# Optimization experiments

Measured on AMD Instinct MI355X. Metric: run time of the kernel, lower is better.

The kernel has to match this reference:

```python
import jax, jax.numpy as jnp
import numpy as np

COMMITMENT_COST = 0.25


def setup_inputs() -> dict:
    key = jax.random.key(0)
    k1, k2 = jax.random.split(key)
    n_embeddings, embedding_dim = 1024, 256
    x = jax.random.normal(k1, (32, 2048, embedding_dim), dtype=jnp.float32)
    r = 1.0 / n_embeddings
    embedding = jax.random.uniform(k2, (n_embeddings, embedding_dim),
                                   dtype=jnp.float32, minval=-r, maxval=r)
    return {"x": x, "embedding": embedding}


def reference(x, embedding):
    M, D = embedding.shape
    # x is detached before flattening in the original quantize()
    x_flat = jax.lax.stop_gradient(x).reshape(-1, D)  # [N, D]
    distances = (jnp.sum(embedding * embedding, axis=1)
                 + jnp.sum(x_flat * x_flat, axis=1, keepdims=True)
                 - 2.0 * (x_flat @ embedding.T))  # [N, M]
    indices = jnp.argmin(distances, axis=-1)  # [N] int
    quantized = embedding[indices].reshape(x.shape)  # gather + view_as(x)
    # commitment loss: quantized is detached in the loss term
    e_latent_loss = jnp.mean(jnp.square(x - jax.lax.stop_gradient(quantized)))
    loss = COMMITMENT_COST * e_latent_loss
    return quantized, loss, indices
```

## Files before the change

kernel.cpp:

```cpp
#include <hip/hip_runtime.h>

#define N_ROWS   65536
#define D        256
#define D4       64
#define M        1024
#define LOSS_OFF 16777216
#define IDX_OFF  16777217
#define COMMIT_SCALE (0.25f / 16777216.0f)
#define E_SCALE  1024.0f
#define C_SCALE  0.001953125f

typedef _Float16 f16x8 __attribute__((ext_vector_type(8)));
typedef _Float16 f16x4 __attribute__((ext_vector_type(4)));
typedef float    f32x4 __attribute__((ext_vector_type(4)));

__device__ __forceinline__ void async_copy16(const void* g, void* l) {
    __builtin_amdgcn_global_load_lds(
        (const __attribute__((address_space(1))) unsigned int*)g,
        (__attribute__((address_space(3))) unsigned int*)l, 16, 0, 0);
}

__device__ __forceinline__ float np_block128(const float* __restrict__ a, int l) {
    float r0 = __fmul_rn(a[l +   0], a[l +   0]);
    float r1 = __fmul_rn(a[l +  16], a[l +  16]);
    float r2 = __fmul_rn(a[l +  32], a[l +  32]);
    float r3 = __fmul_rn(a[l +  48], a[l +  48]);
    float r4 = __fmul_rn(a[l +  64], a[l +  64]);
    float r5 = __fmul_rn(a[l +  80], a[l +  80]);
    float r6 = __fmul_rn(a[l +  96], a[l +  96]);
    float r7 = __fmul_rn(a[l + 112], a[l + 112]);
    return __fadd_rn(__fadd_rn(__fadd_rn(r0, r1), __fadd_rn(r2, r3)),
                     __fadd_rn(__fadd_rn(r4, r5), __fadd_rn(r6, r7)));
}
__device__ __forceinline__ float np_reduce16(float v) {
    float s = __fadd_rn(v, __shfl_down(v, 8));
    s = __fadd_rn(s, __shfl_down(s, 4));
    s = __fadd_rn(s, __shfl_down(s, 2));
    s = __fadd_rn(s, __shfl_down(s, 1));
    return s;
}

__global__ __launch_bounds__(256) void norms_kernel(
    const float4* __restrict__ x4, const float4* __restrict__ emb4,
    float* __restrict__ bsq, float* __restrict__ esq,
    float* __restrict__ loss_slot) {
    __shared__ float rowbuf[16 * 260];
    const int tid = threadIdx.x;
    const float4* src4;
    float* dst;
    int row0;
    if (blockIdx.x < 4096) {
        row0 = blockIdx.x * 16;
        src4 = x4 + (size_t)row0 * 64;
        dst = bsq + row0;
    } else {
        row0 = (blockIdx.x - 4096) * 16;
        src4 = emb4 + (size_t)row0 * 64;
        dst = esq + row0;
    }
    #pragma unroll
    for (int p = 0; p < 4; ++p) {
        const int f = tid + p * 256;
        const int r = f >> 6, c4 = f & 63;
        *(float4*)&rowbuf[r * 260 + c4 * 4] = src4[f];
    }
    __syncthreads();
    const int l = tid & 15, g = tid >> 4;
    const float* base = &rowbuf[g * 260];
    const float v0 = np_block128(base, l);
    const float v1 = np_block128(base + 128, l);
    const float t0 = np_reduce16(v0);
    const float t1 = np_reduce16(v1);
    if (l == 0) dst[g] = __fadd_rn(t0, t1);
    if (blockIdx.x == 0 && tid == 0) *loss_slot = 0.0f;
}

__global__ __launch_bounds__(256) void esplit_kernel(
    const float4* __restrict__ emb4,
    _Float16* __restrict__ e_hi, _Float16* __restrict__ e_mid) {
    const int f = blockIdx.x * 256 + threadIdx.x;
    const int code = f >> 6, k4 = f & 63;
    const int kc = k4 >> 3, k8 = k4 & 7;
    const int q = k8 >> 1, half = k8 & 1;
    const int jt = code >> 7, cl = code & 127;
    const int cg = cl >> 4, lmc = cl & 15;
    float4 v = emb4[f];
    float a[4] = {v.x * E_SCALE, v.y * E_SCALE, v.z * E_SCALE, v.w * E_SCALE};
    f16x4 hi, mid;
    #pragma unroll
    for (int j = 0; j < 4; ++j) {
        _Float16 h = (_Float16)a[j];
        float r = __fsub_rn(a[j], (float)h);
        hi[j] = h;
        mid[j] = (_Float16)r;
    }
    const size_t ofs = (size_t)kc * 32768 + (size_t)jt * 4096
                     + (size_t)(cg * 64 + q * 16 + lmc) * 8 + half * 4;
    *(f16x4*)&e_hi[ofs]  = hi;
    *(f16x4*)&e_mid[ofs] = mid;
}

__global__ __launch_bounds__(256, 2) void argmin_mfma_kernel(
    const float* __restrict__ x,
    const _Float16* __restrict__ e_hi, const _Float16* __restrict__ e_mid,
    const float* __restrict__ esq, const float* __restrict__ bsq,
    float* __restrict__ idx_out_f, int* __restrict__ idx_out_i) {
    __shared__ __attribute__((aligned(16))) _Float16 buf[2][8192];
    __shared__ float red_d[64][2];
    __shared__ int   red_i[64][2];

    const int tid = threadIdx.x;
    const int w = tid >> 6, lane = tid & 63;
    const int w_row = w >> 1, w_col = w & 1;
    const int lm = lane & 15, q = lane >> 4;
    const int row0 = blockIdx.x * 64;

    f16x8 a_hi[2][8], a_mid[2][8];
    #pragma unroll
    for (int fm = 0; fm < 2; ++fm) {
        const float* xr = x + (size_t)(row0 + w_row * 32 + fm * 16 + lm) * D + q * 8;
        #pragma unroll
        for (int kc = 0; kc < 8; ++kc) {
            float4 v0 = *(const float4*)(xr + kc * 32);
            float4 v1 = *(const float4*)(xr + kc * 32 + 4);
            float e[8] = {v0.x, v0.y, v0.z, v0.w, v1.x, v1.y, v1.z, v1.w};
            #pragma unroll
            for (int j = 0; j < 8; ++j) {
                _Float16 h = (_Float16)e[j];
                float r = __fsub_rn(e[j], (float)h);
                a_hi[fm][kc][j]  = h;
                a_mid[fm][kc][j] = (_Float16)r;
            }
        }
    }
    float bq[2][4];
    #pragma unroll
    for (int fm = 0; fm < 2; ++fm)
        #pragma unroll
        for (int r = 0; r < 4; ++r)
            bq[fm][r] = bsq[row0 + w_row * 32 + fm * 16 + q * 4 + r];

    float best[2][4] = {{3.0e38f, 3.0e38f, 3.0e38f, 3.0e38f},
                        {3.0e38f, 3.0e38f, 3.0e38f, 3.0e38f}};
    int bidx[2][4] = {{0, 0, 0, 0}, {0, 0, 0, 0}};

    auto dma = [&](int c, int bsel) {
        const int jt = c >> 3, kc = c & 7;
        const size_t gofs = (size_t)kc * 65536 + (size_t)jt * 8192
                          + (size_t)w * 2048 + (size_t)lane * 16;
        const char* gh = (const char*)e_hi + gofs;
        const char* gm = (const char*)e_mid + gofs;
        _Float16* lh = &buf[bsel][w * 1024];
        _Float16* lmm = &buf[bsel][4096 + w * 1024];
        async_copy16(gh, lh);
        async_copy16(gh + 1024, lh + 512);
        async_copy16(gm, lmm);
        async_copy16(gm + 1024, lmm + 512);
    };

    dma(0, 0);
    for (int jt = 0; jt < 8; ++jt) {
        const int j0 = jt * 128;
        f32x4 acc[2][4] = {};
        for (int kc = 0; kc < 8; ++kc) {
            const int c = jt * 8 + kc;
            __syncthreads();
            if (c < 63) dma(c + 1, (c + 1) & 1);
            const int bsel = c & 1;
            f16x8 bh[4], bm[4];
            const int lofs = lane * 8;
            #pragma unroll
            for (int fn = 0; fn < 4; ++fn) {
                const int bo = (w_col * 4 + fn) * 512 + lofs;
                bh[fn] = *(const f16x8*)&buf[bsel][bo];
                bm[fn] = *(const f16x8*)&buf[bsel][4096 + bo];
            }
            #pragma unroll
            for (int fm = 0; fm < 2; ++fm)
                #pragma unroll
                for (int fn = 0; fn < 4; ++fn) {
                    acc[fm][fn] = __builtin_amdgcn_mfma_f32_16x16x32_f16(
                        a_hi[fm][kc], bh[fn], acc[fm][fn], 0, 0, 0);
                    acc[fm][fn] = __builtin_amdgcn_mfma_f32_16x16x32_f16(
                        a_mid[fm][kc], bh[fn], acc[fm][fn], 0, 0, 0);
                    acc[fm][fn] = __builtin_amdgcn_mfma_f32_16x16x32_f16(
                        a_hi[fm][kc], bm[fn], acc[fm][fn], 0, 0, 0);
                }
        }
        #pragma unroll
        for (int fn = 0; fn < 4; ++fn) {
            const int j = j0 + w_col * 64 + fn * 16 + lm;
            const float eq = esq[j];
            #pragma unroll
            for (int fm = 0; fm < 2; ++fm)
                #pragma unroll
                for (int r = 0; r < 4; ++r) {
                    const float d = __fsub_rn(__fadd_rn(eq, bq[fm][r]),
                                              acc[fm][fn][r] * C_SCALE);
                    if (d < best[fm][r]) { best[fm][r] = d; bidx[fm][r] = j; }
                }
        }
    }
    #pragma unroll
    for (int fm = 0; fm < 2; ++fm)
        #pragma unroll
        for (int r = 0; r < 4; ++r) {
            float d = best[fm][r]; int i = bidx[fm][r];
            #pragma unroll
            for (int mv = 1; mv <= 8; mv <<= 1) {
                const float d2 = __shfl_xor(d, mv, 64);
                const int   i2 = __shfl_xor(i, mv, 64);
                if (d2 < d || (d2 == d && i2 < i)) { d = d2; i = i2; }
            }
            best[fm][r] = d; bidx[fm][r] = i;
        }
    __syncthreads();
    if (lm == 0) {
        #pragma unroll
        for (int fm = 0; fm < 2; ++fm)
            #pragma unroll
            for (int r = 0; r < 4; ++r) {
                const int rl = w_row * 32 + fm * 16 + q * 4 + r;
                red_d[rl][w_col] = best[fm][r];
                red_i[rl][w_col] = bidx[fm][r];
            }
    }
    __syncthreads();
    if (tid < 64) {
        float d0 = red_d[tid][0]; int i0 = red_i[tid][0];
        const float d1 = red_d[tid][1]; const int i1 = red_i[tid][1];
        if (d1 < d0 || (d1 == d0 && i1 < i0)) { d0 = d1; i0 = i1; }
        idx_out_f[row0 + tid] = (float)i0;
        idx_out_i[row0 + tid] = i0;
    }
}

__global__ __launch_bounds__(256) void gather_loss_kernel(
    const float4* __restrict__ x4, const float4* __restrict__ emb4,
    const int* __restrict__ idx, float4* __restrict__ q4,
    float* __restrict__ loss_slot) {
    const int base = blockIdx.x * 256 + threadIdx.x;
    float acc = 0.0f;
    #pragma unroll
    for (int i = 0; i < 16; ++i) {
        const int f   = base + i * (1024 * 256);
        const int row = f >> 6;
        const int c4  = f & 63;
        const int e   = idx[row];
        float4 qv = emb4[e * D4 + c4];
        float4 xv = x4[f];
        q4[f] = qv;
        const float dx = xv.x - qv.x, dy = xv.y - qv.y;
        const float dz = xv.z - qv.z, dw = xv.w - qv.w;
        acc += dx * dx + dy * dy + dz * dz + dw * dw;
    }
    #pragma unroll
    for (int off = 32; off; off >>= 1) acc += __shfl_down(acc, off, 64);
    __shared__ float wsum[4];
    const int lane = threadIdx.x & 63, w = threadIdx.x >> 6;
    if (lane == 0) wsum[w] = acc;
    __syncthreads();
    if (threadIdx.x == 0) {
        atomicAdd(loss_slot, (wsum[0] + wsum[1] + wsum[2] + wsum[3]) * COMMIT_SCALE);
    }
}

extern "C" void kernel_launch(void* const* d_in, const int* in_sizes, int n_in,
                              void* d_out, int out_size, void* d_ws, size_t ws_size,
                              hipStream_t stream) {
    const float* x   = (const float*)d_in[0];
    const float* emb = (const float*)d_in[1];
    float* out = (float*)d_out;
    float*    bsq  = (float*)d_ws;
    float*    esq  = bsq + N_ROWS;
    int*      idx  = (int*)(esq + M);
    _Float16* e_hi = (_Float16*)(idx + N_ROWS);
    _Float16* e_mid = e_hi + (size_t)M * D;

    norms_kernel<<<4096 + M / 16, 256, 0, stream>>>((const float4*)x,
                                                    (const float4*)emb,
                                                    bsq, esq, out + LOSS_OFF);
    esplit_kernel<<<M * D / 4 / 256, 256, 0, stream>>>((const float4*)emb,
                                                       e_hi, e_mid);
    argmin_mfma_kernel<<<N_ROWS / 64, 256, 0, stream>>>(x, e_hi, e_mid,
                                                        esq, bsq,
                                                        out + IDX_OFF, idx);
    gather_loss_kernel<<<1024, 256, 0, stream>>>((const float4*)x,
                                                 (const float4*)emb, idx,
                                                 (float4*)out, out + LOSS_OFF);
}
```

Measured before the change: 248.5 us.

## Triple-buffer codebook DMA with explicit vmcnt waits and stage esq in LDS

Moves the codebook tile prefetch from double to triple buffering, so chunk c+2 is issued while chunk c is computed. The __syncthreads is replaced by explicit s_waitcnt vmcnt(4)/s_barrier sequences so only the oldest DMA must complete before each step. MFMA blocks are raised in wave priority with s_setprio, and the esq table is staged in LDS instead of being read from global memory in the epilogue. The extra buffer increases LDS use, which may limit occupancy, and the hand-written waitcnt logic relies on an exact count of outstanding loads.

```diff
diff --git a/kernel.cpp b/kernel.cpp
--- a/kernel.cpp
+++ b/kernel.cpp
@@ -105,7 +105,8 @@
     const _Float16* __restrict__ e_hi, const _Float16* __restrict__ e_mid,
     const float* __restrict__ esq, const float* __restrict__ bsq,
     float* __restrict__ idx_out_f, int* __restrict__ idx_out_i) {
-    __shared__ __attribute__((aligned(16))) _Float16 buf[2][8192];
+    __shared__ __attribute__((aligned(16))) _Float16 buf[3][8192];
+    __shared__ float esq_lds[1024];
     __shared__ float red_d[64][2];
     __shared__ int   red_i[64][2];
 
@@ -115,6 +116,20 @@
     const int lm = lane & 15, q = lane >> 4;
     const int row0 = blockIdx.x * 64;
 
+    auto dma = [&](int c, int s) {
+        const int jt = c >> 3, kc = c & 7;
+        const size_t gofs = (size_t)kc * 65536 + (size_t)jt * 8192
+                          + (size_t)w * 2048 + (size_t)lane * 16;
+        const char* gh = (const char*)e_hi + gofs;
+        const char* gm = (const char*)e_mid + gofs;
+        _Float16* lh = &buf[s][w * 1024];
+        _Float16* lmm = &buf[s][4096 + w * 1024];
+        async_copy16(gh, lh);
+        async_copy16(gh + 1024, lh + 512);
+        async_copy16(gm, lmm);
+        async_copy16(gm + 1024, lmm + 512);
+    };
+
     f16x8 a_hi[2][8], a_mid[2][8];
     #pragma unroll
     for (int fm = 0; fm < 2; ++fm) {
@@ -140,41 +155,43 @@
         for (int r = 0; r < 4; ++r)
             bq[fm][r] = bsq[row0 + w_row * 32 + fm * 16 + q * 4 + r];
 
+    *(float4*)&esq_lds[tid * 4] = ((const float4*)esq)[tid];
+
+    asm volatile("s_waitcnt vmcnt(0)" ::: "memory");
+
+    dma(0, 0);
+    dma(1, 1);
+
     float best[2][4] = {{3.0e38f, 3.0e38f, 3.0e38f, 3.0e38f},
                         {3.0e38f, 3.0e38f, 3.0e38f, 3.0e38f}};
     int bidx[2][4] = {{0, 0, 0, 0}, {0, 0, 0, 0}};
 
-    auto dma = [&](int c, int bsel) {
-        const int jt = c >> 3, kc = c & 7;
-        const size_t gofs = (size_t)kc * 65536 + (size_t)jt * 8192
-                          + (size_t)w * 2048 + (size_t)lane * 16;
-        const char* gh = (const char*)e_hi + gofs;
-        const char* gm = (const char*)e_mid + gofs;
-        _Float16* lh = &buf[bsel][w * 1024];
-        _Float16* lmm = &buf[bsel][4096 + w * 1024];
-        async_copy16(gh, lh);
-        async_copy16(gh + 1024, lh + 512);
-        async_copy16(gm, lmm);
-        async_copy16(gm + 1024, lmm + 512);
-    };
-
-    dma(0, 0);
+    int rslot = 0;
     for (int jt = 0; jt < 8; ++jt) {
         const int j0 = jt * 128;
         f32x4 acc[2][4] = {};
         for (int kc = 0; kc < 8; ++kc) {
             const int c = jt * 8 + kc;
-            __syncthreads();
-            if (c < 63) dma(c + 1, (c + 1) & 1);
-            const int bsel = c & 1;
+            if (c < 63)
+                asm volatile("s_waitcnt vmcnt(4) lgkmcnt(0)\n\t"
+                             "s_barrier" ::: "memory");
+            else
+                asm volatile("s_waitcnt vmcnt(0) lgkmcnt(0)\n\t"
+                             "s_barrier" ::: "memory");
+            __builtin_amdgcn_sched_barrier(0);
+            if (c <= 61) {
+                int ws = rslot + 2; if (ws >= 3) ws -= 3;
+                dma(c + 2, ws);
+            }
             f16x8 bh[4], bm[4];
             const int lofs = lane * 8;
             #pragma unroll
             for (int fn = 0; fn < 4; ++fn) {
                 const int bo = (w_col * 4 + fn) * 512 + lofs;
-                bh[fn] = *(const f16x8*)&buf[bsel][bo];
-                bm[fn] = *(const f16x8*)&buf[bsel][4096 + bo];
-            }
+                bh[fn] = *(const f16x8*)&buf[rslot][bo];
+                bm[fn] = *(const f16x8*)&buf[rslot][4096 + bo];
+            }
+            __builtin_amdgcn_s_setprio(1);
             #pragma unroll
             for (int fm = 0; fm < 2; ++fm)
                 #pragma unroll
@@ -186,11 +203,13 @@
                     acc[fm][fn] = __builtin_amdgcn_mfma_f32_16x16x32_f16(
                         a_hi[fm][kc], bm[fn], acc[fm][fn], 0, 0, 0);
                 }
+            __builtin_amdgcn_s_setprio(0);
+            rslot = (rslot == 2) ? 0 : rslot + 1;
         }
         #pragma unroll
         for (int fn = 0; fn < 4; ++fn) {
             const int j = j0 + w_col * 64 + fn * 16 + lm;
-            const float eq = esq[j];
+            const float eq = esq_lds[j];
             #pragma unroll
             for (int fm = 0; fm < 2; ++fm)
                 #pragma unroll
```

Result: no change. 248.8 us (+0.1%).

## Software-pipeline codebook loads against MFMA and move x-mid fragments to LDS

Applied to the files above, without the earlier changes.

Restructures the argmin MFMA loop so LDS fragment loads for chunk k overlap the MFMAs of chunk k-1, with the distance epilogue deferred and fused into the next tile's first step. The x low-order (mid) fragments move from registers to shared memory, and the codebook norms are staged in LDS. A manual waitcnt plus barrier replaces __syncthreads, and s_setprio raises priority around the MFMA bursts. The aim is to hide LDS and DMA latency and to lower register pressure for occupancy. The cost is extra LDS traffic and footprint, plus hand-placed waits that are fragile.

```diff
diff --git a/kernel.cpp b/kernel.cpp
--- a/kernel.cpp
+++ b/kernel.cpp
@@ -106,101 +106,149 @@
     const float* __restrict__ esq, const float* __restrict__ bsq,
     float* __restrict__ idx_out_f, int* __restrict__ idx_out_i) {
     __shared__ __attribute__((aligned(16))) _Float16 buf[2][8192];
-    __shared__ float red_d[64][2];
-    __shared__ int   red_i[64][2];
+    __shared__ __attribute__((aligned(16))) _Float16 amid[2][8192];
+    __shared__ float esq_lds[1024];
 
     const int tid = threadIdx.x;
     const int w = tid >> 6, lane = tid & 63;
     const int w_row = w >> 1, w_col = w & 1;
     const int lm = lane & 15, q = lane >> 4;
     const int row0 = blockIdx.x * 64;
-
-    f16x8 a_hi[2][8], a_mid[2][8];
-    #pragma unroll
-    for (int fm = 0; fm < 2; ++fm) {
-        const float* xr = x + (size_t)(row0 + w_row * 32 + fm * 16 + lm) * D + q * 8;
-        #pragma unroll
-        for (int kc = 0; kc < 8; ++kc) {
-            float4 v0 = *(const float4*)(xr + kc * 32);
-            float4 v1 = *(const float4*)(xr + kc * 32 + 4);
-            float e[8] = {v0.x, v0.y, v0.z, v0.w, v1.x, v1.y, v1.z, v1.w};
-            #pragma unroll
-            for (int j = 0; j < 8; ++j) {
-                _Float16 h = (_Float16)e[j];
-                float r = __fsub_rn(e[j], (float)h);
-                a_hi[fm][kc][j]  = h;
-                a_mid[fm][kc][j] = (_Float16)r;
-            }
-        }
-    }
-    float bq[2][4];
-    #pragma unroll
-    for (int fm = 0; fm < 2; ++fm)
-        #pragma unroll
-        for (int r = 0; r < 4; ++r)
-            bq[fm][r] = bsq[row0 + w_row * 32 + fm * 16 + q * 4 + r];
-
-    float best[2][4] = {{3.0e38f, 3.0e38f, 3.0e38f, 3.0e38f},
-                        {3.0e38f, 3.0e38f, 3.0e38f, 3.0e38f}};
-    int bidx[2][4] = {{0, 0, 0, 0}, {0, 0, 0, 0}};
-
-    auto dma = [&](int c, int bsel) {
-        const int jt = c >> 3, kc = c & 7;
-        const size_t gofs = (size_t)kc * 65536 + (size_t)jt * 8192
+    const int lofs = lane * 8;
+
+    auto dma = [&](int jtn, int kcn, int s) {
+        const size_t gofs = (size_t)kcn * 65536 + (size_t)jtn * 8192
                           + (size_t)w * 2048 + (size_t)lane * 16;
         const char* gh = (const char*)e_hi + gofs;
         const char* gm = (const char*)e_mid + gofs;
-        _Float16* lh = &buf[bsel][w * 1024];
-        _Float16* lmm = &buf[bsel][4096 + w * 1024];
+        _Float16* lh  = &buf[s][w * 1024];
+        _Float16* lmm = &buf[s][4096 + w * 1024];
         async_copy16(gh, lh);
         async_copy16(gh + 1024, lh + 512);
         async_copy16(gm, lmm);
         async_copy16(gm + 1024, lmm + 512);
     };
 
-    dma(0, 0);
+    dma(0, 0, 0);
+
+    f16x8 a_hi[2][8];
+    #pragma unroll
+    for (int fm = 0; fm < 2; ++fm) {
+        const float* xr = x + (size_t)(row0 + w_row * 32 + fm * 16 + lm) * D + q * 8;
+        #pragma unroll
+        for (int kc = 0; kc < 8; ++kc) {
+            float4 v0 = *(const float4*)(xr + kc * 32);
+            float4 v1 = *(const float4*)(xr + kc * 32 + 4);
+            float e[8] = {v0.x, v0.y, v0.z, v0.w, v1.x, v1.y, v1.z, v1.w};
+            f16x8 hi, md;
+            #pragma unroll
+            for (int j = 0; j < 8; ++j) {
+                _Float16 h = (_Float16)e[j];
+                float r = __fsub_rn(e[j], (float)h);
+                hi[j] = h;
+                md[j] = (_Float16)r;
+            }
+            a_hi[fm][kc] = hi;
+            if (w_col == 0)
+                *(f16x8*)&amid[w_row][(fm * 8 + kc) * 512 + lofs] = md;
+        }
+    }
+    float bq[2][4];
+    #pragma unroll
+    for (int fm = 0; fm < 2; ++fm)
+        #pragma unroll
+        for (int r = 0; r < 4; ++r)
+            bq[fm][r] = bsq[row0 + w_row * 32 + fm * 16 + q * 4 + r];
+
+    *(float4*)&esq_lds[tid * 4] = ((const float4*)esq)[tid];
+
+    asm volatile("s_waitcnt vmcnt(0)" ::: "memory");
+
+    float best[2][4] = {{3.0e38f, 3.0e38f, 3.0e38f, 3.0e38f},
+                        {3.0e38f, 3.0e38f, 3.0e38f, 3.0e38f}};
+    int bidx[2][4] = {{0, 0, 0, 0}, {0, 0, 0, 0}};
+    f32x4 acc[2][4] = {};
+    f16x8 bh[2][4], bm[2][4], am[2][2];
+
+#define MFMA_TRIPLES(P, KCP)                                                  \
+    do {                                                                      \
+        __builtin_amdgcn_s_setprio(1);                                        \
+        _Pragma("unroll")                                                     \
+        for (int fm = 0; fm < 2; ++fm)                                        \
+            _Pragma("unroll")                                                 \
+            for (int fn = 0; fn < 4; ++fn) {                                  \
+                acc[fm][fn] = __builtin_amdgcn_mfma_f32_16x16x32_f16(         \
+                    a_hi[fm][(KCP)], bh[(P)][fn], acc[fm][fn], 0, 0, 0);      \
+                acc[fm][fn] = __builtin_amdgcn_mfma_f32_16x16x32_f16(         \
+                    am[(P)][fm],     bh[(P)][fn], acc[fm][fn], 0, 0, 0);      \
+                acc[fm][fn] = __builtin_amdgcn_mfma_f32_16x16x32_f16(         \
+                    a_hi[fm][(KCP)], bm[(P)][fn], acc[fm][fn], 0, 0, 0);      \
+            }                                                                 \
+        __builtin_amdgcn_s_setprio(0);                                        \
+    } while (0)
+
+#define EPILOGUE(JT)                                                          \
+    do {                                                                      \
+        const int j0e = (JT) * 128;                                           \
+        _Pragma("unroll")                                                     \
+        for (int fn = 0; fn < 4; ++fn) {                                      \
+            const int j = j0e + w_col * 64 + fn * 16 + lm;                    \
+            const float eq = esq_lds[j];                                      \
+            _Pragma("unroll")                                                 \
+            for (int fm = 0; fm < 2; ++fm)                                    \
+                _Pragma("unroll")                                             \
+                for (int r = 0; r < 4; ++r) {                                 \
+                    const float d = __fsub_rn(__fadd_rn(eq, bq[fm][r]),       \
+                                              acc[fm][fn][r] * C_SCALE);      \
+                    if (d < best[fm][r]) { best[fm][r] = d; bidx[fm][r] = j; }\
+                }                                                             \
+        }                                                                     \
+        _Pragma("unroll")                                                     \
+        for (int fm = 0; fm < 2; ++fm)                                        \
+            _Pragma("unroll")                                                 \
+            for (int fn = 0; fn < 4; ++fn)                                    \
+                _Pragma("unroll")                                             \
+                for (int r = 0; r < 4; ++r) acc[fm][fn][r] = 0.0f;            \
+    } while (0)
+
     for (int jt = 0; jt < 8; ++jt) {
-        const int j0 = jt * 128;
-        f32x4 acc[2][4] = {};
+        #pragma unroll
         for (int kc = 0; kc < 8; ++kc) {
-            const int c = jt * 8 + kc;
-            __syncthreads();
-            if (c < 63) dma(c + 1, (c + 1) & 1);
-            const int bsel = c & 1;
-            f16x8 bh[4], bm[4];
-            const int lofs = lane * 8;
-            #pragma unroll
-            for (int fn = 0; fn < 4; ++fn) {
-                const int bo = (w_col * 4 + fn) * 512 + lofs;
-                bh[fn] = *(const f16x8*)&buf[bsel][bo];
-                bm[fn] = *(const f16x8*)&buf[bsel][4096 + bo];
-            }
-            #pragma unroll
-            for (int fm = 0; fm < 2; ++fm)
+            asm volatile("s_waitcnt vmcnt(0) lgkmcnt(0)\n\t"
+                         "s_barrier" ::: "memory");
+            __builtin_amdgcn_sched_barrier(0);
+            if (kc < 7)       dma(jt, kc + 1, (kc + 1) & 1);
+            else if (jt < 7)  dma(jt + 1, 0, 0);
+            {
+                const int P = kc & 1;
                 #pragma unroll
                 for (int fn = 0; fn < 4; ++fn) {
-                    acc[fm][fn] = __builtin_amdgcn_mfma_f32_16x16x32_f16(
-                        a_hi[fm][kc], bh[fn], acc[fm][fn], 0, 0, 0);
-                    acc[fm][fn] = __builtin_amdgcn_mfma_f32_16x16x32_f16(
-                        a_mid[fm][kc], bh[fn], acc[fm][fn], 0, 0, 0);
-                    acc[fm][fn] = __builtin_amdgcn_mfma_f32_16x16x32_f16(
-                        a_hi[fm][kc], bm[fn], acc[fm][fn], 0, 0, 0);
+                    const int bo = (w_col * 4 + fn) * 512 + lofs;
+                    bh[P][fn] = *(const f16x8*)&buf[P][bo];
+                    bm[P][fn] = *(const f16x8*)&buf[P][4096 + bo];
                 }
+                #pragma unroll
+                for (int fm = 0; fm < 2; ++fm)
+                    am[P][fm] = *(const f16x8*)
+                        &amid[w_row][(fm * 8 + kc) * 512 + lofs];
+            }
+            if (kc == 0) {
+                if (jt) {
+                    MFMA_TRIPLES(1, 7);
+                    EPILOGUE(jt - 1);
+                }
+            } else {
+                MFMA_TRIPLES((kc - 1) & 1, kc - 1);
+            }
         }
-        #pragma unroll
-        for (int fn = 0; fn < 4; ++fn) {
-            const int j = j0 + w_col * 64 + fn * 16 + lm;
-            const float eq = esq[j];
-            #pragma unroll
-            for (int fm = 0; fm < 2; ++fm)
-                #pragma unroll
-                for (int r = 0; r < 4; ++r) {
-                    const float d = __fsub_rn(__fadd_rn(eq, bq[fm][r]),
-                                              acc[fm][fn][r] * C_SCALE);
-                    if (d < best[fm][r]) { best[fm][r] = d; bidx[fm][r] = j; }
-                }
-        }
-    }
+    }
+    asm volatile("s_waitcnt lgkmcnt(0)" ::: "memory");
+    __builtin_amdgcn_sched_barrier(0);
+    MFMA_TRIPLES(1, 7);
+    EPILOGUE(7);
+#undef MFMA_TRIPLES
+#undef EPILOGUE
+
     #pragma unroll
     for (int fm = 0; fm < 2; ++fm)
         #pragma unroll
@@ -214,6 +262,8 @@
             }
             best[fm][r] = d; bidx[fm][r] = i;
         }
+    float* red_d = (float*)&buf[0][0];
+    int*   red_i = (int*)&buf[0][256];
     __syncthreads();
     if (lm == 0) {
         #pragma unroll
@@ -221,14 +271,14 @@
             #pragma unroll
             for (int r = 0; r < 4; ++r) {
                 const int rl = w_row * 32 + fm * 16 + q * 4 + r;
-                red_d[rl][w_col] = best[fm][r];
-                red_i[rl][w_col] = bidx[fm][r];
+                red_d[rl * 2 + w_col] = best[fm][r];
+                red_i[rl * 2 + w_col] = bidx[fm][r];
             }
     }
     __syncthreads();
     if (tid < 64) {
-        float d0 = red_d[tid][0]; int i0 = red_i[tid][0];
-        const float d1 = red_d[tid][1]; const int i1 = red_i[tid][1];
+        float d0 = red_d[tid * 2]; int i0 = red_i[tid * 2];
+        const float d1 = red_d[tid * 2 + 1]; const int i1 = red_i[tid * 2 + 1];
         if (d1 < d0 || (d1 == d0 && i1 < i0)) { d0 = d1; i0 = i1; }
         idx_out_f[row0 + tid] = (float)i0;
         idx_out_i[row0 + tid] = i0;
```

Result: slower. 323.3 us (+30.1%).

## Fold embedding split into norms kernel and read codebook directly from global

Applied to the files above, without the earlier changes.

Merges the fp16 hi/mid codebook split into the norms kernel, removing one kernel launch. The argmin kernel no longer double-buffers codebook tiles into LDS with async copies and per-chunk barriers; each wave loads its B fragments straight from global memory, relying on L2/L1 since every block reads the same 1 MB codebook. The embedding squared norms are staged in LDS once per block. This removes the barriers and LDS traffic but exposes global-load latency directly in front of the MFMAs, and each wave pair now issues redundant codebook loads.

```diff
diff --git a/kernel.cpp b/kernel.cpp
--- a/kernel.cpp
+++ b/kernel.cpp
@@ -13,12 +13,6 @@
 typedef _Float16 f16x8 __attribute__((ext_vector_type(8)));
 typedef _Float16 f16x4 __attribute__((ext_vector_type(4)));
 typedef float    f32x4 __attribute__((ext_vector_type(4)));
-
-__device__ __forceinline__ void async_copy16(const void* g, void* l) {
-    __builtin_amdgcn_global_load_lds(
-        (const __attribute__((address_space(1))) unsigned int*)g,
-        (__attribute__((address_space(3))) unsigned int*)l, 16, 0, 0);
-}
 
 __device__ __forceinline__ float np_block128(const float* __restrict__ a, int l) {
     float r0 = __fmul_rn(a[l +   0], a[l +   0]);
@@ -43,13 +37,15 @@
 __global__ __launch_bounds__(256) void norms_kernel(
     const float4* __restrict__ x4, const float4* __restrict__ emb4,
     float* __restrict__ bsq, float* __restrict__ esq,
+    _Float16* __restrict__ e_hi, _Float16* __restrict__ e_mid,
     float* __restrict__ loss_slot) {
     __shared__ float rowbuf[16 * 260];
     const int tid = threadIdx.x;
     const float4* src4;
     float* dst;
     int row0;
-    if (blockIdx.x < 4096) {
+    const bool is_emb = blockIdx.x >= 4096;
+    if (!is_emb) {
         row0 = blockIdx.x * 16;
         src4 = x4 + (size_t)row0 * 64;
         dst = bsq + row0;
@@ -73,31 +69,34 @@
     const float t1 = np_reduce16(v1);
     if (l == 0) dst[g] = __fadd_rn(t0, t1);
     if (blockIdx.x == 0 && tid == 0) *loss_slot = 0.0f;
-}
-
-__global__ __launch_bounds__(256) void esplit_kernel(
-    const float4* __restrict__ emb4,
-    _Float16* __restrict__ e_hi, _Float16* __restrict__ e_mid) {
-    const int f = blockIdx.x * 256 + threadIdx.x;
-    const int code = f >> 6, k4 = f & 63;
-    const int kc = k4 >> 3, k8 = k4 & 7;
-    const int q = k8 >> 1, half = k8 & 1;
-    const int jt = code >> 7, cl = code & 127;
-    const int cg = cl >> 4, lmc = cl & 15;
-    float4 v = emb4[f];
-    float a[4] = {v.x * E_SCALE, v.y * E_SCALE, v.z * E_SCALE, v.w * E_SCALE};
-    f16x4 hi, mid;
-    #pragma unroll
-    for (int j = 0; j < 4; ++j) {
-        _Float16 h = (_Float16)a[j];
-        float r = __fsub_rn(a[j], (float)h);
-        hi[j] = h;
-        mid[j] = (_Float16)r;
-    }
-    const size_t ofs = (size_t)kc * 32768 + (size_t)jt * 4096
-                     + (size_t)(cg * 64 + q * 16 + lmc) * 8 + half * 4;
-    *(f16x4*)&e_hi[ofs]  = hi;
-    *(f16x4*)&e_mid[ofs] = mid;
+
+    if (is_emb) {
+        #pragma unroll
+        for (int p = 0; p < 4; ++p) {
+            const int f = tid + p * 256;
+            const int r = f >> 6, k4 = f & 63;
+            const int code = row0 + r;
+            const int kc = k4 >> 3, k8 = k4 & 7;
+            const int q = k8 >> 1, half = k8 & 1;
+            const int jt = code >> 7, cl = code & 127;
+            const int cg = cl >> 4, lmc = cl & 15;
+            float4 v = *(const float4*)&rowbuf[r * 260 + k4 * 4];
+            float a[4] = {v.x * E_SCALE, v.y * E_SCALE,
+                          v.z * E_SCALE, v.w * E_SCALE};
+            f16x4 hi, mid;
+            #pragma unroll
+            for (int j = 0; j < 4; ++j) {
+                _Float16 h = (_Float16)a[j];
+                float rr = __fsub_rn(a[j], (float)h);
+                hi[j] = h;
+                mid[j] = (_Float16)rr;
+            }
+            const size_t ofs = (size_t)kc * 32768 + (size_t)jt * 4096
+                             + (size_t)(cg * 64 + q * 16 + lmc) * 8 + half * 4;
+            *(f16x4*)&e_hi[ofs]  = hi;
+            *(f16x4*)&e_mid[ofs] = mid;
+        }
+    }
 }
 
 __global__ __launch_bounds__(256, 2) void argmin_mfma_kernel(
@@ -105,7 +104,7 @@
     const _Float16* __restrict__ e_hi, const _Float16* __restrict__ e_mid,
     const float* __restrict__ esq, const float* __restrict__ bsq,
     float* __restrict__ idx_out_f, int* __restrict__ idx_out_i) {
-    __shared__ __attribute__((aligned(16))) _Float16 buf[2][8192];
+    __shared__ float esq_lds[1024];
     __shared__ float red_d[64][2];
     __shared__ int   red_i[64][2];
 
@@ -140,40 +139,25 @@
         for (int r = 0; r < 4; ++r)
             bq[fm][r] = bsq[row0 + w_row * 32 + fm * 16 + q * 4 + r];
 
+    *(float4*)&esq_lds[tid * 4] = ((const float4*)esq)[tid];
+    __syncthreads();
+
     float best[2][4] = {{3.0e38f, 3.0e38f, 3.0e38f, 3.0e38f},
                         {3.0e38f, 3.0e38f, 3.0e38f, 3.0e38f}};
     int bidx[2][4] = {{0, 0, 0, 0}, {0, 0, 0, 0}};
 
-    auto dma = [&](int c, int bsel) {
-        const int jt = c >> 3, kc = c & 7;
-        const size_t gofs = (size_t)kc * 65536 + (size_t)jt * 8192
-                          + (size_t)w * 2048 + (size_t)lane * 16;
-        const char* gh = (const char*)e_hi + gofs;
-        const char* gm = (const char*)e_mid + gofs;
-        _Float16* lh = &buf[bsel][w * 1024];
-        _Float16* lmm = &buf[bsel][4096 + w * 1024];
-        async_copy16(gh, lh);
-        async_copy16(gh + 1024, lh + 512);
-        async_copy16(gm, lmm);
-        async_copy16(gm + 1024, lmm + 512);
-    };
-
-    dma(0, 0);
+    const int fofs = (w_col * 4) * 512 + lane * 8;
     for (int jt = 0; jt < 8; ++jt) {
         const int j0 = jt * 128;
         f32x4 acc[2][4] = {};
+        #pragma unroll
         for (int kc = 0; kc < 8; ++kc) {
-            const int c = jt * 8 + kc;
-            __syncthreads();
-            if (c < 63) dma(c + 1, (c + 1) & 1);
-            const int bsel = c & 1;
+            const size_t cb = (size_t)kc * 32768 + (size_t)jt * 4096 + fofs;
             f16x8 bh[4], bm[4];
-            const int lofs = lane * 8;
             #pragma unroll
             for (int fn = 0; fn < 4; ++fn) {
-                const int bo = (w_col * 4 + fn) * 512 + lofs;
-                bh[fn] = *(const f16x8*)&buf[bsel][bo];
-                bm[fn] = *(const f16x8*)&buf[bsel][4096 + bo];
+                bh[fn] = *(const f16x8*)&e_hi[cb + fn * 512];
+                bm[fn] = *(const f16x8*)&e_mid[cb + fn * 512];
             }
             #pragma unroll
             for (int fm = 0; fm < 2; ++fm)
@@ -190,7 +174,7 @@
         #pragma unroll
         for (int fn = 0; fn < 4; ++fn) {
             const int j = j0 + w_col * 64 + fn * 16 + lm;
-            const float eq = esq[j];
+            const float eq = esq_lds[j];
             #pragma unroll
             for (int fm = 0; fm < 2; ++fm)
                 #pragma unroll
@@ -279,9 +263,8 @@
 
     norms_kernel<<<4096 + M / 16, 256, 0, stream>>>((const float4*)x,
                                                     (const float4*)emb,
-                                                    bsq, esq, out + LOSS_OFF);
-    esplit_kernel<<<M * D / 4 / 256, 256, 0, stream>>>((const float4*)emb,
-                                                       e_hi, e_mid);
+                                                    bsq, esq, e_hi, e_mid,
+                                                    out + LOSS_OFF);
     argmin_mfma_kernel<<<N_ROWS / 64, 256, 0, stream>>>(x, e_hi, e_mid,
                                                         esq, bsq,
                                                         out + IDX_OFF, idx);
```

New measurement: 267.7 us. 1.08x slower.
